# Performance work log

Hardware: AMD Instinct MI355X
Metric: run time of the kernel (lower is better)

Reference implementation:

```python
import jax, jax.numpy as jnp
import numpy as np

B, S, P, D, H, L, DF, O = 8, 1024, 128, 256, 4, 4, 1024, 10
DH = D // H  # 64
EPS = 1e-5


def get_positional_embeddings(seq_len, d):
    i = np.arange(seq_len, dtype=np.float64)[:, None]
    j = np.arange(d, dtype=np.float64)[None, :]
    even = np.sin(i / 10000 ** (j / d))
    odd = np.cos(i / 10000 ** ((j - 1) / d))
    return jnp.asarray(np.where(j % 2 == 0, even, odd), dtype=jnp.float32)


def layernorm(x, g, b):
    m = jnp.mean(x, axis=-1, keepdims=True)
    v = jnp.mean(jnp.square(x - m), axis=-1, keepdims=True)
    return (x - m) * jax.lax.rsqrt(v + EPS) * g + b


def setup_inputs() -> dict:
    key = jax.random.key(0)
    ks = jax.random.split(key, 20)
    w = lambda k, shp: (jax.random.normal(k, shp, dtype=jnp.float32) * 0.02)
    return {
        "images": jax.random.normal(ks[0], (B, S, P), dtype=jnp.float32),
        "Wp": w(ks[1], (D, P)), "bp": jnp.zeros((D,), jnp.float32),
        "cls": jax.random.uniform(ks[2], (1, D), dtype=jnp.float32),
        "pos": get_positional_embeddings(S + 1, D),
        "ln1_g": jnp.ones((L, D), jnp.float32), "ln1_b": jnp.zeros((L, D), jnp.float32),
        "Wq": w(ks[3], (L, H, DH, DH)), "bq": jnp.zeros((L, H, DH), jnp.float32),
        "Wk": w(ks[4], (L, H, DH, DH)), "bk": jnp.zeros((L, H, DH), jnp.float32),
        "Wv": w(ks[5], (L, H, DH, DH)), "bv": jnp.zeros((L, H, DH), jnp.float32),
        "ln2_g": jnp.ones((L, D), jnp.float32), "ln2_b": jnp.zeros((L, D), jnp.float32),
        "W1": w(ks[6], (L, DF, D)), "b1": jnp.zeros((L, DF), jnp.float32),
        "W2": w(ks[7], (L, D, DF)), "b2": jnp.zeros((L, D), jnp.float32),
        "Wo": w(ks[8], (O, D)), "bo": jnp.zeros((O,), jnp.float32),
    }


def msa(x, Wq, bq, Wk, bk, Wv, bv):
    b, s, _ = x.shape
    xh = x.reshape(b, s, H, DH)  # split heads along feature dim
    # torch Linear: y = x @ W.T + b, per head
    q = jnp.einsum("bshd,hed->bhse", xh, Wq) + bq[None, :, None, :]
    k = jnp.einsum("bshd,hed->bhse", xh, Wk) + bk[None, :, None, :]
    v = jnp.einsum("bshd,hed->bhse", xh, Wv) + bv[None, :, None, :]
    scores = jnp.einsum("bhqd,bhkd->bhqk", q, k) / (DH ** 0.5)
    attn = jax.nn.softmax(scores, axis=-1)
    out = jnp.einsum("bhqk,bhkd->bhqd", attn, v)  # [b,h,s,dh]
    return out.transpose(0, 2, 1, 3).reshape(b, s, D)  # hstack heads


def reference(images, Wp, bp, cls, pos, ln1_g, ln1_b, Wq, bq, Wk, bk, Wv, bv,
              ln2_g, ln2_b, W1, b1, W2, b2, Wo, bo):
    tokens = jnp.einsum("bsp,dp->bsd", images, Wp) + bp
    x = jnp.concatenate([jnp.broadcast_to(cls[None], (B, 1, D)), tokens], axis=1)
    x = x + pos[None]
    for l in range(L):
        x = x + msa(layernorm(x, ln1_g[l], ln1_b[l]), Wq[l], bq[l], Wk[l], bk[l], Wv[l], bv[l])
        h = layernorm(x, ln2_g[l], ln2_b[l])
        h = jax.nn.gelu(jnp.einsum("bsd,fd->bsf", h, W1[l]) + b1[l], approximate=False)
        x = x + jnp.einsum("bsf,df->bsd", h, W2[l]) + b2[l]
    logits = x[:, 0] @ Wo.T + bo
    return jax.nn.softmax(logits, axis=-1)
```

## Files before the change

kernel.cpp:

```cpp
#include <hip/hip_runtime.h>
#include <hip/hip_bf16.h>
#include <cmath>

constexpr int B  = 8;
constexpr int S  = 1024;
constexpr int P  = 128;
constexpr int D  = 256;
constexpr int H  = 4;
constexpr int L  = 4;
constexpr int DF = 1024;
constexpr int O  = 10;
constexpr int DH = D / H;
constexpr int SP = S + 1;
constexpr int N  = B * SP;
constexpr int KVPAD = 1088;

typedef short bf16x8 __attribute__((ext_vector_type(8)));
typedef float f32x4 __attribute__((ext_vector_type(4)));
typedef float f32x16 __attribute__((ext_vector_type(16)));
typedef unsigned int u32;
typedef unsigned short u16;

static __device__ __forceinline__ u16 f2b(float f) {
    __hip_bfloat16 h = __float2bfloat16(f);
    u16 u; __builtin_memcpy(&u, &h, 2);
    return u;
}
static __device__ __forceinline__ float b2f(u16 u) {
    u32 uu = (u32)u << 16; float f; __builtin_memcpy(&f, &uu, 4);
    return f;
}
static __device__ __forceinline__ u32 pk2(float a, float b) {
    return (u32)f2b(a) | ((u32)f2b(b) << 16);
}
static __device__ __forceinline__ void gload_lds16(const void* g, void* l) {
    __builtin_amdgcn_global_load_lds((const __attribute__((address_space(1))) unsigned int*)g,
                                     (__attribute__((address_space(3))) unsigned int*)l, 16, 0, 0);
}

__global__ void cvt_all(const float* __restrict__ s0, u16* __restrict__ d0, int n0,
                        const float* __restrict__ s1, u16* __restrict__ d1, int n1,
                        const float* __restrict__ s2, u16* __restrict__ d2, int n2,
                        const float* __restrict__ s3, u16* __restrict__ d3, int n3) {
    int y = blockIdx.y;
    const float* s = y == 0 ? s0 : y == 1 ? s1 : y == 2 ? s2 : s3;
    u16* d = y == 0 ? d0 : y == 1 ? d1 : y == 2 ? d2 : d3;
    int n = y == 0 ? n0 : y == 1 ? n1 : y == 2 ? n2 : n3;
    int i = blockIdx.x * 256 + threadIdx.x;
    if (i < n) {
        float4 v = ((const float4*)s)[i];
        ushort4 o;
        o.x = f2b(v.x); o.y = f2b(v.y); o.z = f2b(v.z); o.w = f2b(v.w);
        ((ushort4*)d)[i] = o;
    }
}

__global__ void build_wqkv(const float* __restrict__ Wq, const float* __restrict__ bq,
                           const float* __restrict__ Wk, const float* __restrict__ bk,
                           const float* __restrict__ Wv, const float* __restrict__ bv,
                           u16* __restrict__ Wout, float* __restrict__ bout) {
    int r = blockIdx.x, l = blockIdx.y, c = threadIdx.x;
    int sec = r >> 8;
    int ef = r & 255, h = ef >> 6, e = ef & 63;
    const float* W  = sec == 0 ? Wq : sec == 1 ? Wk : Wv;
    const float* bi = sec == 0 ? bq : sec == 1 ? bk : bv;
    float scale = sec == 0 ? 0.125f * 1.4426950408889634f : 1.0f;
    float val = ((c >> 6) == h) ? W[(((size_t)l * H + h) * 64 + e) * 64 + (c & 63)] * scale : 0.f;
    Wout[((size_t)l * 768 + r) * 256 + c] = f2b(val);
    if (c == 0) bout[(size_t)l * 768 + r] = bi[((size_t)l * H + h) * 64 + e] * scale;
}

template <int EPI>
__global__ __launch_bounds__(256) void gemm_bf16(
        const u16* __restrict__ X, const u16* __restrict__ W,
        const float* __restrict__ bias, const float* __restrict__ pos,
        float* __restrict__ Yf, u16* __restrict__ Yb,
        int M, int F, int K, int kLen) {
    __shared__ u16 Al[2][64 * 64];
    __shared__ u16 Bl[2][128 * 64];
    const int t = threadIdx.x;
    const int m0 = blockIdx.y * 64, f0 = blockIdx.x * 128;
    const int w = t >> 6, l = t & 63;
    const int wm = w >> 1, wn = w & 1;
    const int q = l & 15, g = l >> 4;
    const int kOff = blockIdx.z * kLen;
    const int lr8 = l >> 3, lp = l & 7;

    f32x4 acc[2][4];
    const f32x4 zz = {0.f, 0.f, 0.f, 0.f};
#pragma unroll
    for (int i = 0; i < 2; ++i)
#pragma unroll
        for (int j = 0; j < 4; ++j) acc[i][j] = zz;

    auto stage = [&](int sb, int kbase) {
#pragma unroll
        for (int i = 0; i < 2; ++i) {
            int ca = w + 4 * i;
            int row = ca * 8 + lr8;
            int j = lp ^ (row & 7);
            gload_lds16(X + (size_t)(m0 + row) * K + kbase + j * 8, &Al[sb][ca * 512]);
        }
#pragma unroll
        for (int i = 0; i < 4; ++i) {
            int cb = w + 4 * i;
            int row = cb * 8 + lr8;
            int j = lp ^ (row & 7);
            gload_lds16(W + (size_t)(f0 + row) * K + kbase + j * 8, &Bl[sb][cb * 512]);
        }
    };

    const int nt = kLen / 64;
    stage(0, kOff);
    __syncthreads();
    int sb = 0;
    for (int ts = 0; ts < nt; ++ts) {
        if (ts + 1 < nt) stage(sb ^ 1, kOff + (ts + 1) * 64);
#pragma unroll
        for (int kk = 0; kk < 2; ++kk) {
            bf16x8 a[2], bfr[4];
#pragma unroll
            for (int fi = 0; fi < 2; ++fi) {
                int row = wm * 32 + fi * 16 + q;
                a[fi] = *(const bf16x8*)&Al[sb][row * 64 + (((kk * 4 + g) ^ (row & 7)) * 8)];
            }
#pragma unroll
            for (int fj = 0; fj < 4; ++fj) {
                int row = wn * 64 + fj * 16 + q;
                bfr[fj] = *(const bf16x8*)&Bl[sb][row * 64 + (((kk * 4 + g) ^ (row & 7)) * 8)];
            }
#pragma unroll
            for (int fi = 0; fi < 2; ++fi)
#pragma unroll
                for (int fj = 0; fj < 4; ++fj)
                    acc[fi][fj] = __builtin_amdgcn_mfma_f32_16x16x32_bf16(a[fi], bfr[fj], acc[fi][fj], 0, 0, 0);
        }
        __syncthreads();
        sb ^= 1;
    }

#pragma unroll
    for (int fi = 0; fi < 2; ++fi) {
#pragma unroll
        for (int r = 0; r < 4; ++r) {
            int m = m0 + wm * 32 + fi * 16 + g * 4 + r;
            if (m >= M) continue;
#pragma unroll
            for (int fj = 0; fj < 4; ++fj) {
                int f = f0 + wn * 64 + fj * 16 + q;
                float val = acc[fi][fj][r];
                if constexpr (EPI == 0) {
                    val += bias[f];
                    int s = m & 1023, bb = m >> 10;
                    size_t n = (size_t)bb * SP + s + 1;
                    Yf[n * D + f] = val + pos[(size_t)(s + 1) * D + f];
                } else if constexpr (EPI == 1) {
                    val += bias[f];
                    float gel = 0.5f * val * (1.0f + erff(val * 0.70710678118654752f));
                    Yb[(size_t)m * F + f] = f2b(gel);
                } else if constexpr (EPI == 3) {
                    val += bias[f];
                    Yb[(size_t)m * F + f] = f2b(val);
                } else {
                    Yb[(size_t)blockIdx.z * M * F + (size_t)m * F + f] = f2b(val);
                }
            }
        }
    }
}

__global__ void transpose_v(const u16* __restrict__ qkv, u16* __restrict__ VTg) {
    __shared__ u16 tile[64][70];
    int bh = blockIdx.y, t0 = blockIdx.x * 64;
    int b = bh >> 2, h = bh & 3;
    int t = threadIdx.x;
    int r = t >> 3, c8 = (t & 7) * 8;
#pragma unroll
    for (int it = 0; it < 2; ++it) {
        int sp = t0 + it * 32 + r; if (sp > S) sp = S;
        uint4 v = *(const uint4*)(qkv + ((size_t)b * SP + sp) * 768 + 512 + h * 64 + c8);
        u32* dst = (u32*)&tile[it * 32 + r][c8];
        const u32* pv = (const u32*)&v;
#pragma unroll
        for (int k = 0; k < 4; ++k) dst[k] = pv[k];
    }
    __syncthreads();
#pragma unroll
    for (int it = 0; it < 2; ++it) {
        int d = it * 32 + (t >> 3);
        int spc = (t & 7) * 8;
        u16 tmp[8];
#pragma unroll
        for (int j = 0; j < 8; ++j) tmp[j] = tile[spc + j][d];
        *(uint4*)(VTg + ((size_t)bh * 64 + d) * KVPAD + t0 + spc) = *(const uint4*)tmp;
    }
}

__global__ void ln_first(const float* __restrict__ cls, const float* __restrict__ pos,
                         const float* __restrict__ gw, const float* __restrict__ bw,
                         float* __restrict__ x, u16* __restrict__ dst) {
    int row = blockIdx.x * 4 + (threadIdx.x >> 6);
    int l = threadIdx.x & 63;
    float4 v;
    if ((row % SP) == 0) {
        float4 c = *(const float4*)(cls + l * 4);
        float4 pp = *(const float4*)(pos + l * 4);
        v.x = c.x + pp.x; v.y = c.y + pp.y; v.z = c.z + pp.z; v.w = c.w + pp.w;
        *(float4*)(x + (size_t)row * D + l * 4) = v;
    } else {
        v = *(const float4*)(x + (size_t)row * D + l * 4);
    }
    float s = v.x + v.y + v.z + v.w;
    for (int off = 32; off; off >>= 1) s += __shfl_xor(s, off, 64);
    float mean = s * (1.0f / D);
    float dx0 = v.x - mean, dx1 = v.y - mean, dx2 = v.z - mean, dx3 = v.w - mean;
    float sq = dx0 * dx0 + dx1 * dx1 + dx2 * dx2 + dx3 * dx3;
    for (int off = 32; off; off >>= 1) sq += __shfl_xor(sq, off, 64);
    float rs = rsqrtf(sq * (1.0f / D) + 1e-5f);
    float4 gv = *(const float4*)(gw + l * 4);
    float4 bv = *(const float4*)(bw + l * 4);
    ushort4 o;
    o.x = f2b(dx0 * rs * gv.x + bv.x);
    o.y = f2b(dx1 * rs * gv.y + bv.y);
    o.z = f2b(dx2 * rs * gv.z + bv.z);
    o.w = f2b(dx3 * rs * gv.w + bv.w);
    *(ushort4*)(dst + (size_t)row * D + l * 4) = o;
}

__global__ __launch_bounds__(512, 4) void attn_stage(const u16* __restrict__ qkv,
                                                     const u16* __restrict__ VTg,
                                                     u16* __restrict__ opart,
                                                     float* __restrict__ lsum,
                                                     int nqt) {
    const int qg = blockIdx.x, bh = blockIdx.y, quarter = blockIdx.z;
    const int h4 = bh & 3, b = bh >> 2;
    const int t = threadIdx.x;
    const int wv = t >> 6, l = t & 63;
    const int col = l & 31, hh = l >> 5;

    __shared__ u16 Kl[5 * 64 * 64];
    __shared__ u16 Vl[5 * 64 * 64];

    const int kv_start = quarter * 256;
    const int kv_len = (quarter == 3) ? (SP - 768) : 256;
    const int ntiles = (kv_len + 63) >> 6;

    const int qt = qg * 8 + wv;
    const int q0w = qt * 32;

    bf16x8 qf[4];
    {
        int qr = q0w + col; if (qr > S) qr = S;
        const u16* qp = qkv + ((size_t)b * SP + qr) * 768 + h4 * 64 + hh * 8;
#pragma unroll
        for (int c = 0; c < 4; ++c) qf[c] = *(const bf16x8*)(qp + c * 16);
    }

    {
        const int rloc = wv * 8 + (l >> 3);
        const int j = (l & 7) ^ (((rloc >> 3) ^ rloc) & 7);
        for (int tt = 0; tt < ntiles; ++tt) {
            int krow = kv_start + tt * 64 + rloc; if (krow > S) krow = S;
            gload_lds16(qkv + ((size_t)b * SP + krow) * 768 + 256 + h4 * 64 + j * 8,
                        &Kl[(tt * 8 + wv) * 512]);
            gload_lds16(VTg + ((size_t)bh * 64 + rloc) * KVPAD + kv_start + tt * 64 + j * 8,
                        &Vl[(tt * 8 + wv) * 512]);
        }
    }
    __syncthreads();
    if (qt >= nqt) return;

    const int swA = ((col >> 3) ^ col) & 7;
    const int swB = swA ^ 4;

    f32x16 o0, o1;
#pragma unroll
    for (int r = 0; r < 16; ++r) { o0[r] = 0.f; o1[r] = 0.f; }
    float l_run = 0.f;

    for (int tile = 0; tile < ntiles; ++tile) {
        const int kv0 = tile * 64;
        const u16* Kt = &Kl[tile * 4096];
        const u16* Vt = &Vl[tile * 4096];

        f32x16 s0, s1;
#pragma unroll
        for (int r = 0; r < 16; ++r) { s0[r] = 0.f; s1[r] = 0.f; }
        __builtin_amdgcn_s_setprio(1);
#pragma unroll
        for (int c = 0; c < 4; ++c) {
            bf16x8 k0 = *(const bf16x8*)&Kt[col * 64 + (((2 * c + hh) ^ swA) * 8)];
            bf16x8 k1 = *(const bf16x8*)&Kt[(32 + col) * 64 + (((2 * c + hh) ^ swB) * 8)];
            s0 = __builtin_amdgcn_mfma_f32_32x32x16_bf16(k0, qf[c], s0, 0, 0, 0);
            s1 = __builtin_amdgcn_mfma_f32_32x32x16_bf16(k1, qf[c], s1, 0, 0, 0);
        }
        __builtin_amdgcn_s_setprio(0);

        float p[32];
#pragma unroll
        for (int r = 0; r < 16; ++r) { p[r] = s0[r]; p[16 + r] = s1[r]; }

        if (kv0 + 64 > kv_len) {
#pragma unroll
            for (int kvs = 0; kvs < 2; ++kvs)
#pragma unroll
                for (int r = 0; r < 16; ++r) {
                    int kvloc = kvs * 32 + (r & 3) + 8 * (r >> 2) + 4 * hh;
                    if (kv0 + kvloc >= kv_len) p[kvs * 16 + r] = -1e30f;
                }
        }

#pragma unroll
        for (int j = 0; j < 32; ++j) p[j] = exp2f(p[j]);
        {
            float t16[16];
#pragma unroll
            for (int j = 0; j < 16; ++j) t16[j] = p[2 * j] + p[2 * j + 1];
#pragma unroll
            for (int j = 0; j < 8; ++j) t16[j] = t16[j] + t16[j + 8];
#pragma unroll
            for (int j = 0; j < 4; ++j) t16[j] = t16[j] + t16[j + 4];
            l_run += (t16[0] + t16[1]) + (t16[2] + t16[3]);
        }

        __builtin_amdgcn_s_setprio(1);
#pragma unroll
        for (int kvs = 0; kvs < 2; ++kvs) {
            u32 pk[8];
#pragma unroll
            for (int i = 0; i < 8; ++i) pk[i] = pk2(p[kvs * 16 + 2 * i], p[kvs * 16 + 2 * i + 1]);
            u32 ex[4];
#pragma unroll
            for (int kk = 0; kk < 4; ++kk) {
                const int k = (kk < 2) ? kk : kk + 2;
                u32 send = hh ? pk[k] : pk[k + 2];
                ex[kk] = (u32)__shfl_xor((int)send, 32);
            }
#pragma unroll
            for (int cc = 0; cc < 2; ++cc) {
                union { u32 u[4]; bf16x8 v; } pa;
                u32 e0 = ex[cc * 2], e1 = ex[cc * 2 + 1];
                pa.u[0] = hh ? e0 : pk[4 * cc];
                pa.u[1] = hh ? e1 : pk[4 * cc + 1];
                pa.u[2] = hh ? pk[4 * cc + 2] : e0;
                pa.u[3] = hh ? pk[4 * cc + 3] : e1;
                int lch = kvs * 4 + cc * 2 + hh;
                bf16x8 v0 = *(const bf16x8*)&Vt[col * 64 + ((lch ^ swA) * 8)];
                bf16x8 v1 = *(const bf16x8*)&Vt[(32 + col) * 64 + ((lch ^ swB) * 8)];
                o0 = __builtin_amdgcn_mfma_f32_32x32x16_bf16(pa.v, v0, o0, 0, 0, 0);
                o1 = __builtin_amdgcn_mfma_f32_32x32x16_bf16(pa.v, v1, o1, 0, 0, 0);
            }
        }
        __builtin_amdgcn_s_setprio(0);
    }

    float l_full = l_run + __shfl_xor(l_run, 32);
    const size_t obase = ((size_t)quarter * 32 + bh) * SP;
#pragma unroll
    for (int r = 0; r < 16; ++r) {
        int qrow = (r & 3) + 8 * (r >> 2) + 4 * hh;
        int qq = q0w + qrow;
        if (qq < SP) {
            opart[(obase + qq) * 64 + col]      = f2b(o0[r]);
            opart[(obase + qq) * 64 + 32 + col] = f2b(o1[r]);
        }
    }
    if (l < 32) {
        int qq = q0w + l;
        if (qq < SP) lsum[obase + qq] = l_full;
    }
}

__global__ void combine_ln2(const u16* __restrict__ opart, const float* __restrict__ lsum,
                            const float* __restrict__ gw, const float* __restrict__ bw,
                            float* __restrict__ x, u16* __restrict__ lnb) {
    int row = blockIdx.x * 4 + (threadIdx.x >> 6);
    int l = threadIdx.x & 63;
    int b = row / SP, qq = row % SP;
    int h = l >> 4, d0 = (l * 4) & 63;
    int bh = b * 4 + h;
    float csum = 0.f, a0 = 0.f, a1 = 0.f, a2 = 0.f, a3 = 0.f;
#pragma unroll
    for (int i = 0; i < 4; ++i) {
        size_t idx = ((size_t)i * 32 + bh) * SP + qq;
        csum += lsum[idx];
        ushort4 ov = *(const ushort4*)&opart[idx * 64 + d0];
        a0 += b2f(ov.x); a1 += b2f(ov.y); a2 += b2f(ov.z); a3 += b2f(ov.w);
    }
    float inv = 1.0f / csum;
    float4 xv = *(const float4*)(x + (size_t)row * D + l * 4);
    xv.x += a0 * inv; xv.y += a1 * inv; xv.z += a2 * inv; xv.w += a3 * inv;
    *(float4*)(x + (size_t)row * D + l * 4) = xv;

    float s = xv.x + xv.y + xv.z + xv.w;
    for (int off = 32; off; off >>= 1) s += __shfl_xor(s, off, 64);
    float mean = s * (1.0f / D);
    float dx0 = xv.x - mean, dx1 = xv.y - mean, dx2 = xv.z - mean, dx3 = xv.w - mean;
    float sq = dx0 * dx0 + dx1 * dx1 + dx2 * dx2 + dx3 * dx3;
    for (int off = 32; off; off >>= 1) sq += __shfl_xor(sq, off, 64);
    float rs = rsqrtf(sq * (1.0f / D) + 1e-5f);
    float4 gv = *(const float4*)(gw + l * 4);
    float4 bv = *(const float4*)(bw + l * 4);
    ushort4 o;
    o.x = f2b(dx0 * rs * gv.x + bv.x);
    o.y = f2b(dx1 * rs * gv.y + bv.y);
    o.z = f2b(dx2 * rs * gv.z + bv.z);
    o.w = f2b(dx3 * rs * gv.w + bv.w);
    *(ushort4*)(lnb + (size_t)row * D + l * 4) = o;
}

__global__ void combine2_ln1(const u16* __restrict__ Pkb, const float* __restrict__ b2,
                             const float* __restrict__ gw, const float* __restrict__ bw,
                             float* __restrict__ x, u16* __restrict__ lnb) {
    int row = blockIdx.x * 4 + (threadIdx.x >> 6);
    int l = threadIdx.x & 63;
    ushort4 p0 = *(const ushort4*)(Pkb + (size_t)row * D + l * 4);
    ushort4 p1 = *(const ushort4*)(Pkb + (size_t)N * D + (size_t)row * D + l * 4);
    float4 bv2 = *(const float4*)(b2 + l * 4);
    float4 xv = *(const float4*)(x + (size_t)row * D + l * 4);
    xv.x += b2f(p0.x) + b2f(p1.x) + bv2.x;
    xv.y += b2f(p0.y) + b2f(p1.y) + bv2.y;
    xv.z += b2f(p0.z) + b2f(p1.z) + bv2.z;
    xv.w += b2f(p0.w) + b2f(p1.w) + bv2.w;
    *(float4*)(x + (size_t)row * D + l * 4) = xv;

    float s = xv.x + xv.y + xv.z + xv.w;
    for (int off = 32; off; off >>= 1) s += __shfl_xor(s, off, 64);
    float mean = s * (1.0f / D);
    float dx0 = xv.x - mean, dx1 = xv.y - mean, dx2 = xv.z - mean, dx3 = xv.w - mean;
    float sq = dx0 * dx0 + dx1 * dx1 + dx2 * dx2 + dx3 * dx3;
    for (int off = 32; off; off >>= 1) sq += __shfl_xor(sq, off, 64);
    float rs = rsqrtf(sq * (1.0f / D) + 1e-5f);
    float4 gv = *(const float4*)(gw + l * 4);
    float4 bv = *(const float4*)(bw + l * 4);
    ushort4 o;
    o.x = f2b(dx0 * rs * gv.x + bv.x);
    o.y = f2b(dx1 * rs * gv.y + bv.y);
    o.z = f2b(dx2 * rs * gv.z + bv.z);
    o.w = f2b(dx3 * rs * gv.w + bv.w);
    *(ushort4*)(lnb + (size_t)row * D + l * 4) = o;
}

__global__ void tail_ln(const u16* __restrict__ opart, const float* __restrict__ lsum,
                        const float* __restrict__ x,
                        const float* __restrict__ g2, const float* __restrict__ b2w,
                        float* __restrict__ xc, float* __restrict__ lnc) {
    __shared__ float red[4];
    const int b = blockIdx.x, t = threadIdx.x;
    const int h = t >> 6, dl = t & 63;
    float csum = 0.f, a = 0.f;
#pragma unroll
    for (int i = 0; i < 4; ++i) {
        size_t idx = ((size_t)i * 32 + b * 4 + h) * SP;
        csum += lsum[idx];
        a += b2f(opart[idx * 64 + dl]);
    }
    float xv = x[(size_t)b * SP * D + t] + a / csum;
    xc[b * D + t] = xv;

    float s = xv;
    for (int off = 32; off; off >>= 1) s += __shfl_xor(s, off, 64);
    if ((t & 63) == 0) red[t >> 6] = s;
    __syncthreads();
    float mean = (red[0] + red[1] + red[2] + red[3]) * (1.0f / D);
    float dx = xv - mean;
    float sq = dx * dx;
    for (int off = 32; off; off >>= 1) sq += __shfl_xor(sq, off, 64);
    __syncthreads();
    if ((t & 63) == 0) red[t >> 6] = sq;
    __syncthreads();
    float var = (red[0] + red[1] + red[2] + red[3]) * (1.0f / D);
    lnc[b * D + t] = dx * rsqrtf(var + 1e-5f) * g2[t] + b2w[t];
}

__global__ void tail_mlp1(const float* __restrict__ lnc,
                          const u16* __restrict__ W1l, const float* __restrict__ b1l,
                          float* __restrict__ midc) {
    __shared__ float ln[256];
    const int fc = blockIdx.x, b = blockIdx.y, t = threadIdx.x;
    ln[t] = lnc[b * D + t];
    __syncthreads();
    const int f = fc * 128 + (t >> 1);
    const int half = t & 1;
    const u16* wr = W1l + (size_t)f * D + half * 128;
    const float* lp = &ln[half * 128];
    float acc = 0.f;
#pragma unroll
    for (int d = 0; d < 128; d += 8) {
        bf16x8 wv = *(const bf16x8*)(wr + d);
        const u16* wu = (const u16*)&wv;
#pragma unroll
        for (int j = 0; j < 8; ++j) acc += lp[d + j] * b2f(wu[j]);
    }
    acc += __shfl_xor(acc, 1);
    if (half == 0) {
        float v = acc + b1l[f];
        midc[b * DF + f] = 0.5f * v * (1.0f + erff(v * 0.70710678118654752f));
    }
}

__global__ void tail_mlp2(const float* __restrict__ midc,
                          const u16* __restrict__ W2l, const float* __restrict__ b2l,
                          const float* __restrict__ xc, float* __restrict__ xc2) {
    __shared__ float mh[1024];
    const int dc = blockIdx.x, b = blockIdx.y, t = threadIdx.x;
#pragma unroll
    for (int i = 0; i < 4; ++i) mh[t + i * 256] = midc[b * DF + t + i * 256];
    __syncthreads();
    const int dout = dc * 32 + (t >> 3);
    const int oct = t & 7;
    const u16* wr = W2l + (size_t)dout * DF + oct * 128;
    const float* mp = &mh[oct * 128];
    float acc = 0.f;
#pragma unroll
    for (int f = 0; f < 128; f += 8) {
        bf16x8 wv = *(const bf16x8*)(wr + f);
        const u16* wu = (const u16*)&wv;
#pragma unroll
        for (int j = 0; j < 8; ++j) acc += mp[f + j] * b2f(wu[j]);
    }
    acc += __shfl_xor(acc, 1);
    acc += __shfl_xor(acc, 2);
    acc += __shfl_xor(acc, 4);
    if (oct == 0) xc2[b * D + dout] = xc[b * D + dout] + acc + b2l[dout];
}

__global__ void head_kernel(const float* __restrict__ xc,
                            const float* __restrict__ Wo,
                            const float* __restrict__ bo,
                            float* __restrict__ out) {
    __shared__ float logits[B][O];
    int t = threadIdx.x;
    if (t < B * O) {
        int b = t / O, o = t % O;
        const float* xr = xc + (size_t)b * D;
        float acc = bo[o];
        for (int d = 0; d < D; ++d) acc += xr[d] * Wo[(size_t)o * D + d];
        logits[b][o] = acc;
    }
    __syncthreads();
    if (t < B) {
        float mx = -1e30f;
        for (int o = 0; o < O; ++o) mx = fmaxf(mx, logits[t][o]);
        float s = 0.f, e[O];
        for (int o = 0; o < O; ++o) { e[o] = expf(logits[t][o] - mx); s += e[o]; }
        float inv = 1.0f / s;
        for (int o = 0; o < O; ++o) out[t * O + o] = e[o] * inv;
    }
}

extern "C" void kernel_launch(void* const* d_in, const int* in_sizes, int n_in,
                              void* d_out, int out_size, void* d_ws, size_t ws_size,
                              hipStream_t stream) {
    const float* images = (const float*)d_in[0];
    const float* Wp     = (const float*)d_in[1];
    const float* bp     = (const float*)d_in[2];
    const float* cls    = (const float*)d_in[3];
    const float* pos    = (const float*)d_in[4];
    const float* ln1_g  = (const float*)d_in[5];
    const float* ln1_b  = (const float*)d_in[6];
    const float* Wq     = (const float*)d_in[7];
    const float* bq     = (const float*)d_in[8];
    const float* Wk     = (const float*)d_in[9];
    const float* bk     = (const float*)d_in[10];
    const float* Wv     = (const float*)d_in[11];
    const float* bv     = (const float*)d_in[12];
    const float* ln2_g  = (const float*)d_in[13];
    const float* ln2_b  = (const float*)d_in[14];
    const float* W1     = (const float*)d_in[15];
    const float* b1     = (const float*)d_in[16];
    const float* W2     = (const float*)d_in[17];
    const float* b2     = (const float*)d_in[18];
    const float* Wo     = (const float*)d_in[19];
    const float* bo     = (const float*)d_in[20];
    float* out = (float*)d_out;

    auto align256 = [](size_t v) { return (v + 255) & ~(size_t)255; };
    char* p = (char*)d_ws;
    float* x      = (float*)p; p += align256((size_t)N * D * 4);
    u16* lnb      = (u16*)p;   p += align256((size_t)N * D * 2);
    u16* qkvbuf   = (u16*)p;   p += align256((size_t)(N + 128) * 768 * 2);
    char* midop   = p;         p += align256((size_t)N * DF * 2);
    u16* Pkb      = (u16*)p;   p += align256((size_t)2 * N * D * 2);
    float* lsum   = (float*)p; p += align256((size_t)4 * 32 * SP * 4);
    u16* VTg      = (u16*)p;   p += align256((size_t)32 * 64 * KVPAD * 2);
    u16* imgb     = (u16*)p;   p += align256((size_t)B * S * P * 2);
    u16* Wpb      = (u16*)p;   p += align256((size_t)D * P * 2);
    u16* W1b      = (u16*)p;   p += align256((size_t)L * DF * D * 2);
    u16* W2b      = (u16*)p;   p += align256((size_t)L * D * DF * 2);
    u16* Wqkvb    = (u16*)p;   p += align256((size_t)L * 768 * 256 * 2);
    float* bqkvf  = (float*)p; p += align256((size_t)L * 768 * 4);
    float* xc     = (float*)p; p += align256((size_t)B * D * 4);
    float* lnc    = (float*)p; p += align256((size_t)B * D * 4);
    float* midc   = (float*)p; p += align256((size_t)B * DF * 4);
    float* xc2    = (float*)p; p += align256((size_t)B * D * 4);
    u16* mid      = (u16*)midop;
    u16* opart    = (u16*)midop;

    cvt_all<<<dim3(1024, 4), 256, 0, stream>>>(
        images, imgb, B * S * P / 4,
        Wp, Wpb, D * P / 4,
        W1, W1b, L * DF * D / 4,
        W2, W2b, L * D * DF / 4);
    build_wqkv<<<dim3(768, L), 256, 0, stream>>>(Wq, bq, Wk, bk, Wv, bv, Wqkvb, bqkvf);

    gemm_bf16<0><<<dim3(2, 128, 1), 256, 0, stream>>>(
        imgb, Wpb, bp, pos, x, nullptr, B * S, D, P, P);
    ln_first<<<N / 4, 256, 0, stream>>>(cls, pos, ln1_g, ln1_b, x, lnb);

    for (int l = 0; l < 3; ++l) {
        gemm_bf16<3><<<dim3(6, 129, 1), 256, 0, stream>>>(
            lnb, Wqkvb + (size_t)l * 768 * 256, bqkvf + (size_t)l * 768,
            nullptr, nullptr, qkvbuf, N, 768, D, D);
        transpose_v<<<dim3(17, 32), 256, 0, stream>>>(qkvbuf, VTg);
        attn_stage<<<dim3(5, 32, 4), 512, 0, stream>>>(qkvbuf, VTg, opart, lsum, 33);
        combine_ln2<<<N / 4, 256, 0, stream>>>(opart, lsum, ln2_g + l * D, ln2_b + l * D, x, lnb);
        gemm_bf16<1><<<dim3(8, 129, 1), 256, 0, stream>>>(
            lnb, W1b + (size_t)l * DF * D, b1 + (size_t)l * DF,
            nullptr, nullptr, mid, N, DF, D, D);
        gemm_bf16<4><<<dim3(2, 129, 2), 256, 0, stream>>>(
            mid, W2b + (size_t)l * D * DF, nullptr, nullptr, nullptr, Pkb, N, D, DF, DF / 2);
        combine2_ln1<<<N / 4, 256, 0, stream>>>(Pkb, b2 + (size_t)l * D,
                                                ln1_g + (l + 1) * D, ln1_b + (l + 1) * D, x, lnb);
    }

    {
        const int l = 3;
        gemm_bf16<3><<<dim3(6, 129, 1), 256, 0, stream>>>(
            lnb, Wqkvb + (size_t)l * 768 * 256, bqkvf + (size_t)l * 768,
            nullptr, nullptr, qkvbuf, N, 768, D, D);
        transpose_v<<<dim3(17, 32), 256, 0, stream>>>(qkvbuf, VTg);
        attn_stage<<<dim3(1, 32, 4), 512, 0, stream>>>(qkvbuf, VTg, opart, lsum, 1);
        tail_ln<<<B, 256, 0, stream>>>(opart, lsum, x, ln2_g + l * D, ln2_b + l * D, xc, lnc);
        tail_mlp1<<<dim3(8, B), 256, 0, stream>>>(lnc, W1b + (size_t)l * DF * D,
                                                  b1 + (size_t)l * DF, midc);
        tail_mlp2<<<dim3(8, B), 256, 0, stream>>>(midc, W2b + (size_t)l * D * DF,
                                                  b2 + (size_t)l * D, xc, xc2);
        head_kernel<<<1, 256, 0, stream>>>(xc2, Wo, bo, out);
    }
}
```

Measured before the change: 335.0 us.

## Fuse V transpose into QKV GEMM epilogue and remap attention blocks per XCD

The QKV projection epilogue now writes the V section directly in transposed per-head layout, removing the separate transpose_v kernel and its extra read and write of V. The attention launch becomes a 1D grid whose block index is decoded so that blocks sharing the same head and KV quarter map to the same XCD, which is meant to improve L2 reuse of K/V. The transposed stores are 2-byte strided writes, which are poorly coalesced. Padding columns beyond S are no longer written.

```diff
diff --git a/kernel.cpp b/kernel.cpp
--- a/kernel.cpp
+++ b/kernel.cpp
@@ -74,7 +74,7 @@
 __global__ __launch_bounds__(256) void gemm_bf16(
         const u16* __restrict__ X, const u16* __restrict__ W,
         const float* __restrict__ bias, const float* __restrict__ pos,
-        float* __restrict__ Yf, u16* __restrict__ Yb,
+        float* __restrict__ Yf, u16* __restrict__ Yb, u16* __restrict__ Yb2,
         int M, int F, int K, int kLen) {
     __shared__ u16 Al[2][64 * 64];
     __shared__ u16 Bl[2][128 * 64];
@@ -158,41 +158,20 @@
                     val += bias[f];
                     float gel = 0.5f * val * (1.0f + erff(val * 0.70710678118654752f));
                     Yb[(size_t)m * F + f] = f2b(gel);
-                } else if constexpr (EPI == 3) {
+                } else if constexpr (EPI == 4) {
+                    Yb[(size_t)blockIdx.z * M * F + (size_t)m * F + f] = f2b(val);
+                } else {
                     val += bias[f];
-                    Yb[(size_t)m * F + f] = f2b(val);
-                } else {
-                    Yb[(size_t)blockIdx.z * M * F + (size_t)m * F + f] = f2b(val);
+                    if (f0 < 512) {
+                        Yb[(size_t)m * F + f] = f2b(val);
+                    } else {
+                        int bb = m / SP, sp = m % SP;
+                        int dv = (f - 512) & 63, hv = (f - 512) >> 6;
+                        Yb2[(((size_t)bb * H + hv) * 64 + dv) * KVPAD + sp] = f2b(val);
+                    }
                 }
             }
         }
-    }
-}
-
-__global__ void transpose_v(const u16* __restrict__ qkv, u16* __restrict__ VTg) {
-    __shared__ u16 tile[64][70];
-    int bh = blockIdx.y, t0 = blockIdx.x * 64;
-    int b = bh >> 2, h = bh & 3;
-    int t = threadIdx.x;
-    int r = t >> 3, c8 = (t & 7) * 8;
-#pragma unroll
-    for (int it = 0; it < 2; ++it) {
-        int sp = t0 + it * 32 + r; if (sp > S) sp = S;
-        uint4 v = *(const uint4*)(qkv + ((size_t)b * SP + sp) * 768 + 512 + h * 64 + c8);
-        u32* dst = (u32*)&tile[it * 32 + r][c8];
-        const u32* pv = (const u32*)&v;
-#pragma unroll
-        for (int k = 0; k < 4; ++k) dst[k] = pv[k];
-    }
-    __syncthreads();
-#pragma unroll
-    for (int it = 0; it < 2; ++it) {
-        int d = it * 32 + (t >> 3);
-        int spc = (t & 7) * 8;
-        u16 tmp[8];
-#pragma unroll
-        for (int j = 0; j < 8; ++j) tmp[j] = tile[spc + j][d];
-        *(uint4*)(VTg + ((size_t)bh * 64 + d) * KVPAD + t0 + spc) = *(const uint4*)tmp;
     }
 }
 
@@ -231,8 +210,12 @@
                                                      const u16* __restrict__ VTg,
                                                      u16* __restrict__ opart,
                                                      float* __restrict__ lsum,
-                                                     int nqt) {
-    const int qg = blockIdx.x, bh = blockIdx.y, quarter = blockIdx.z;
+                                                     int nqt, int ngq) {
+    const int bid = blockIdx.x;
+    const int xcd = bid & 7, t2 = bid >> 3;
+    const int g128 = xcd + 8 * (t2 / ngq);
+    const int qg = t2 % ngq;
+    const int quarter = g128 >> 5, bh = g128 & 31;
     const int h4 = bh & 3, b = bh >> 2;
     const int t = threadIdx.x;
     const int wv = t >> 6, l = t & 63;
@@ -605,32 +588,31 @@
     build_wqkv<<<dim3(768, L), 256, 0, stream>>>(Wq, bq, Wk, bk, Wv, bv, Wqkvb, bqkvf);
 
     gemm_bf16<0><<<dim3(2, 128, 1), 256, 0, stream>>>(
-        imgb, Wpb, bp, pos, x, nullptr, B * S, D, P, P);
+        imgb, Wpb, bp, pos, x, nullptr, nullptr, B * S, D, P, P);
     ln_first<<<N / 4, 256, 0, stream>>>(cls, pos, ln1_g, ln1_b, x, lnb);
 
     for (int l = 0; l < 3; ++l) {
-        gemm_bf16<3><<<dim3(6, 129, 1), 256, 0, stream>>>(
+        gemm_bf16<5><<<dim3(6, 129, 1), 256, 0, stream>>>(
             lnb, Wqkvb + (size_t)l * 768 * 256, bqkvf + (size_t)l * 768,
-            nullptr, nullptr, qkvbuf, N, 768, D, D);
-        transpose_v<<<dim3(17, 32), 256, 0, stream>>>(qkvbuf, VTg);
-        attn_stage<<<dim3(5, 32, 4), 512, 0, stream>>>(qkvbuf, VTg, opart, lsum, 33);
+            nullptr, nullptr, qkvbuf, VTg, N, 768, D, D);
+        attn_stage<<<640, 512, 0, stream>>>(qkvbuf, VTg, opart, lsum, 33, 5);
         combine_ln2<<<N / 4, 256, 0, stream>>>(opart, lsum, ln2_g + l * D, ln2_b + l * D, x, lnb);
         gemm_bf16<1><<<dim3(8, 129, 1), 256, 0, stream>>>(
             lnb, W1b + (size_t)l * DF * D, b1 + (size_t)l * DF,
-            nullptr, nullptr, mid, N, DF, D, D);
+            nullptr, nullptr, mid, nullptr, N, DF, D, D);
         gemm_bf16<4><<<dim3(2, 129, 2), 256, 0, stream>>>(
-            mid, W2b + (size_t)l * D * DF, nullptr, nullptr, nullptr, Pkb, N, D, DF, DF / 2);
+            mid, W2b + (size_t)l * D * DF, nullptr, nullptr, nullptr, Pkb, nullptr,
+            N, D, DF, DF / 2);
         combine2_ln1<<<N / 4, 256, 0, stream>>>(Pkb, b2 + (size_t)l * D,
                                                 ln1_g + (l + 1) * D, ln1_b + (l + 1) * D, x, lnb);
     }
 
     {
         const int l = 3;
-        gemm_bf16<3><<<dim3(6, 129, 1), 256, 0, stream>>>(
+        gemm_bf16<5><<<dim3(6, 129, 1), 256, 0, stream>>>(
             lnb, Wqkvb + (size_t)l * 768 * 256, bqkvf + (size_t)l * 768,
-            nullptr, nullptr, qkvbuf, N, 768, D, D);
-        transpose_v<<<dim3(17, 32), 256, 0, stream>>>(qkvbuf, VTg);
-        attn_stage<<<dim3(1, 32, 4), 512, 0, stream>>>(qkvbuf, VTg, opart, lsum, 1);
+            nullptr, nullptr, qkvbuf, VTg, N, 768, D, D);
+        attn_stage<<<128, 512, 0, stream>>>(qkvbuf, VTg, opart, lsum, 1, 1);
         tail_ln<<<B, 256, 0, stream>>>(opart, lsum, x, ln2_g + l * D, ln2_b + l * D, xc, lnc);
         tail_mlp1<<<dim3(8, B), 256, 0, stream>>>(lnc, W1b + (size_t)l * DF * D,
                                                   b1 + (size_t)l * DF, midc);
```

Result: slower. 347.9 us (+3.8%).
